# Optimization experiments

Hardware: AMD Instinct MI355X
Metric: run time of the kernel (lower is better)

The kernel has to match this reference:

```python
import jax, jax.numpy as jnp
import numpy as np

EMBED_DIM = 1024
NUM_HEADS = 16
HEAD_DIM = EMBED_DIM // NUM_HEADS
B, T = 4, 2048


def setup_inputs() -> dict:
    key = jax.random.key(0)
    ks = jax.random.split(key, 5)
    s = 1.0 / np.sqrt(EMBED_DIM)
    x = jax.random.normal(ks[0], (B, T, EMBED_DIM), dtype=jnp.float32)
    attention_mask = jnp.ones((B, 1, 1, T), dtype=jnp.int32)
    # torch Linear weights: qkv (3E, E), out (E, E); store transposed for x @ W
    W_qkv = jax.random.uniform(ks[1], (EMBED_DIM, 3 * EMBED_DIM), jnp.float32, -s, s)
    b_qkv = jax.random.uniform(ks[2], (3 * EMBED_DIM,), jnp.float32, -s, s)
    W_out = jax.random.uniform(ks[3], (EMBED_DIM, EMBED_DIM), jnp.float32, -s, s)
    b_out = jax.random.uniform(ks[4], (EMBED_DIM,), jnp.float32, -s, s)
    return {"x": x, "attention_mask": attention_mask,
            "W_qkv": W_qkv, "b_qkv": b_qkv, "W_out": W_out, "b_out": b_out}


def reference(x, attention_mask, W_qkv, b_qkv, W_out, b_out):
    Bq, Tq, E = x.shape
    qkv = x @ W_qkv + b_qkv                              # [B,T,3E]
    qkv = qkv.reshape(Bq, Tq, 3, NUM_HEADS, HEAD_DIM)
    qkv = jnp.transpose(qkv, (2, 0, 3, 1, 4))            # [3,B,H,T,d]
    q, k, v = qkv[0], qkv[1], qkv[2]
    scores = jnp.einsum('bhqd,bhkd->bhqk', q, k) / jnp.sqrt(
        jnp.asarray(HEAD_DIM, x.dtype))                  # [B,H,T,T]
    scores = jnp.where(attention_mask == 0, jnp.asarray(-jnp.inf, x.dtype), scores)
    attn = jax.nn.softmax(scores, axis=-1)
    ctx = jnp.einsum('bhqk,bhkd->bhqd', attn, v)         # [B,H,T,d]
    ctx = jnp.transpose(ctx, (0, 2, 1, 3)).reshape(Bq, Tq, E)
    return ctx @ W_out + b_out
```

## Files before the change

### kernel.cpp

```cpp
#include <hip/hip_runtime.h>
#include <hip/hip_bf16.h>
#include <stdint.h>


typedef __attribute__((ext_vector_type(8))) short short8;
typedef __attribute__((ext_vector_type(4))) float f32x4;
typedef __attribute__((ext_vector_type(16))) float f32x16;
typedef __attribute__((ext_vector_type(4))) unsigned short ushort4_t;
typedef __attribute__((ext_vector_type(8))) unsigned short ushort8_t;

#define SEQ 2048
#define EDIM 1024
#define QSCALE 0.18033688011112042f

__device__ __forceinline__ unsigned short f2bf(float x) {
  union { float f; uint32_t u; } v; v.f = x;
  uint32_t r = v.u + 0x7fffu + ((v.u >> 16) & 1u);
  return (unsigned short)(r >> 16);
}

__device__ __forceinline__ uint32_t cvtpk(float lo, float hi) {
  uint32_t r;
  asm("v_cvt_pk_bf16_f32 %0, %1, %2" : "=v"(r) : "v"(lo), "v"(hi));
  return r;
}

__device__ __forceinline__ float exp2_raw(float x) {
  float r;
  asm("v_exp_f32 %0, %1" : "=v"(r) : "v"(x));
  return r;
}

__device__ __forceinline__ void gload_lds16(const void* g, void* l) {
  typedef __attribute__((address_space(1))) const unsigned int gu32;
  typedef __attribute__((address_space(3))) unsigned int lu32;
  __builtin_amdgcn_global_load_lds((gu32*)g, (lu32*)l, 16, 0, 0);
}

__global__ void k_cvt(const float* __restrict__ in,
                      unsigned short* __restrict__ out, int n8) {
  int i = blockIdx.x * blockDim.x + threadIdx.x;
  if (i >= n8) return;
  const float4* p = ((const float4*)in) + (size_t)i * 2;
  float4 a = p[0], b = p[1];
  ushort8_t v;
  v[0] = f2bf(a.x); v[1] = f2bf(a.y); v[2] = f2bf(a.z); v[3] = f2bf(a.w);
  v[4] = f2bf(b.x); v[5] = f2bf(b.y); v[6] = f2bf(b.z); v[7] = f2bf(b.w);
  ((ushort8_t*)out)[i] = v;
}

__global__ void k_transpose(const float* __restrict__ W,
                            unsigned short* __restrict__ Wt, int K, int N) {
  __shared__ float tile[32][33];
  int c0 = blockIdx.x * 32;
  int r0 = blockIdx.y * 32;
  int tx = threadIdx.x & 31, ty = threadIdx.x >> 5;
#pragma unroll
  for (int i = 0; i < 4; ++i) {
    int r = ty + i * 8;
    tile[r][tx] = W[(size_t)(r0 + r) * N + c0 + tx];
  }
  __syncthreads();
#pragma unroll
  for (int i = 0; i < 4; ++i) {
    int r = ty + i * 8;
    Wt[(size_t)(c0 + r) * K + r0 + tx] = f2bf(tile[tx][r]);
  }
}

template <int EPI, int NBX>
__global__ __launch_bounds__(256, 2) void k_gemm(
    const unsigned short* __restrict__ A, const unsigned short* __restrict__ Bt,
    const float* __restrict__ bias, unsigned short* __restrict__ Qo,
    unsigned short* __restrict__ Ko, unsigned short* __restrict__ VTo,
    float* __restrict__ Out) {
  __shared__ unsigned short As[128 * 32];
  __shared__ unsigned short Bs[128 * 32];
  const int tid = threadIdx.x;
  const int lane = tid & 63, wid = tid >> 6;
  const int wr = wid >> 1, wc = wid & 1;
  const int g = lane >> 4, r = lane & 15;
  const int lid = blockIdx.y * NBX + blockIdx.x;
  const int total = NBX * gridDim.y;
  const int id = (lid & 7) * (total >> 3) + (lid >> 3);
  const int m0 = (id / NBX) * 128, n0 = (id % NBX) * 128;

  f32x4 zero4 = {0.f, 0.f, 0.f, 0.f};
  f32x4 acc[4][4];
#pragma unroll
  for (int mi = 0; mi < 4; ++mi)
#pragma unroll
    for (int ni = 0; ni < 4; ++ni) acc[mi][ni] = zero4;

  for (int kt = 0; kt < 1024; kt += 32) {
#pragma unroll
    for (int i = 0; i < 2; ++i) {
      int seg = i * 256 + tid;
      int row = seg >> 2, sl = seg & 3;
      gload_lds16(A + (size_t)(m0 + row) * 1024 + kt + sl * 8,
                  (char*)As + (i * 256 + wid * 64) * 16);
      gload_lds16(Bt + (size_t)(n0 + row) * 1024 + kt + sl * 8,
                  (char*)Bs + (i * 256 + wid * 64) * 16);
    }
    __syncthreads();
    short8 af[4], bf[4];
#pragma unroll
    for (int mi = 0; mi < 4; ++mi)
      af[mi] = *(const short8*)&As[(wr * 64 + mi * 16 + r) * 32 + g * 8];
#pragma unroll
    for (int ni = 0; ni < 4; ++ni)
      bf[ni] = *(const short8*)&Bs[(wc * 64 + ni * 16 + r) * 32 + g * 8];
#pragma unroll
    for (int mi = 0; mi < 4; ++mi)
#pragma unroll
      for (int ni = 0; ni < 4; ++ni)
        acc[mi][ni] = __builtin_amdgcn_mfma_f32_16x16x32_bf16(
            af[mi], bf[ni], acc[mi][ni], 0, 0, 0);
    __syncthreads();
  }

#pragma unroll
  for (int mi = 0; mi < 4; ++mi) {
#pragma unroll
    for (int ni = 0; ni < 4; ++ni) {
      const int n = n0 + wc * 64 + ni * 16 + r;
      const float bv = bias[n];
      const int mbase = m0 + wr * 64 + mi * 16 + g * 4;
      if (EPI == 0) {
        const int sec = n >> 10, e = n & 1023, h = e >> 6, dd = e & 63;
        const int b = mbase >> 11, t = mbase & 2047;
        if (sec == 2) {
          ushort4_t pk;
#pragma unroll
          for (int j = 0; j < 4; ++j) pk[j] = f2bf(acc[mi][ni][j] + bv);
          *(ushort4_t*)&VTo[(((size_t)b * 16 + h) * 64 + dd) * 2048 + t] = pk;
        } else {
          unsigned short* dst = (sec == 0) ? Qo : Ko;
          const float scl = (sec == 0) ? QSCALE : 1.0f;
#pragma unroll
          for (int j = 0; j < 4; ++j)
            dst[(((size_t)b * 16 + h) * 2048 + t + j) * 64 + dd] =
                f2bf((acc[mi][ni][j] + bv) * scl);
        }
      } else {
#pragma unroll
        for (int j = 0; j < 4; ++j)
          Out[(size_t)(mbase + j) * 1024 + n] = acc[mi][ni][j] + bv;
      }
    }
  }
}

__global__ __launch_bounds__(256, 4) void k_attn(
    const unsigned short* __restrict__ Qg, const unsigned short* __restrict__ Kg,
    const unsigned short* __restrict__ VTg, const int* __restrict__ maskp,
    unsigned short* __restrict__ ctx) {
  __shared__ unsigned short Ks[2][64 * 64];
  __shared__ unsigned short Vs[2][64 * 64];
  const int tid = threadIdx.x, lane = tid & 63, wid = tid >> 6;
  const int q = lane & 31, hi = lane >> 5;
  const int id = blockIdx.x;
  const int slot = id >> 3;
  const int bh = (id & 7) * 8 + (slot >> 4);
  const int b = bh >> 4, h = bh & 15;
  const int q0 = (slot & 15) * 128 + wid * 32;
  const int qr = q0 + q;

  const unsigned short* Qb = Qg + (size_t)bh * SEQ * 64;
  const unsigned short* Kb = Kg + (size_t)bh * SEQ * 64;
  const unsigned short* Vb = VTg + (size_t)bh * 64 * SEQ;
  const int* mb = maskp + b * SEQ;

  const int r0_ = tid >> 3, sl0_ = (tid & 7) ^ (r0_ & 7);
  const int r1_ = (256 + tid) >> 3, sl1_ = ((256 + tid) & 7) ^ (r1_ & 7);
  const unsigned short* kp0 = Kb + r0_ * 64 + sl0_ * 8;
  const unsigned short* kp1 = Kb + r1_ * 64 + sl1_ * 8;
  const unsigned short* vp0 = Vb + (size_t)r0_ * SEQ + sl0_ * 8;
  const unsigned short* vp1 = Vb + (size_t)r1_ * SEQ + sl1_ * 8;
  char* kbase = (char*)Ks[0] + wid * 1024;
  char* vbase = (char*)Vs[0] + wid * 1024;

  auto STAGE = [&](int buf) {
    const int bo = buf * 8192;
    gload_lds16(kp0, kbase + bo);
    gload_lds16(kp1, kbase + bo + 4096);
    gload_lds16(vp0, vbase + bo);
    gload_lds16(vp1, vbase + bo + 4096);
    kp0 += 64 * 64; kp1 += 64 * 64;
    vp0 += 64; vp1 += 64;
  };

  short8 qf[4];
#pragma unroll
  for (int ds = 0; ds < 4; ++ds)
    qf[ds] = *(const short8*)&Qb[(size_t)qr * 64 + ds * 16 + hi * 8];

  short8 onesf;
#pragma unroll
  for (int j = 0; j < 8; ++j) onesf[j] = (short)0x3F80;

  f32x16 z16 = {0.f,0.f,0.f,0.f,0.f,0.f,0.f,0.f,0.f,0.f,0.f,0.f,0.f,0.f,0.f,0.f};
  f32x16 o0 = z16, o1 = z16;
  f32x16 osum = z16;
  const int kb4 = hi * 4;

  STAGE(0);
  const int* mptr = mb + lane;
  int mv = mptr[0];
  mptr += 64;

  for (int t = 0; t < 32; ++t) {
    const int cur = t & 1;
    __syncthreads();
    int mvn = 1;
    if (t < 31) {
      STAGE(cur ^ 1);
      mvn = mptr[0];
      mptr += 64;
    }
    const unsigned long long bits = __ballot(mv != 0);
    mv = mvn;

    const char* KsB = (const char*)Ks[cur];
    const char* VsB = (const char*)Vs[cur];
    f32x16 c0 = z16, c1 = z16;
    __builtin_amdgcn_s_setprio(1);
#pragma unroll
    for (int ds = 0; ds < 4; ++ds) {
      const int sl = ds * 2 + hi;
      short8 ka0 = *(const short8*)(KsB + q * 128 + ((sl ^ (q & 7)) * 16));
      short8 ka1 = *(const short8*)(KsB + (32 + q) * 128 + ((sl ^ (q & 7)) * 16));
      c0 = __builtin_amdgcn_mfma_f32_32x32x16_bf16(ka0, qf[ds], c0, 0, 0, 0);
      c1 = __builtin_amdgcn_mfma_f32_32x32x16_bf16(ka1, qf[ds], c1, 0, 0, 0);
    }
    __builtin_amdgcn_s_setprio(0);

#pragma unroll
    for (int i = 0; i < 16; ++i) {
      c0[i] = exp2_raw(c0[i]);
      c1[i] = exp2_raw(c1[i]);
    }
    if (bits != ~0ull) {
#pragma unroll
      for (int i = 0; i < 16; ++i) {
        const int k0 = (i & 3) + 8 * (i >> 2) + kb4;
        if (!((bits >> k0) & 1)) c0[i] = 0.f;
        if (!((bits >> (k0 + 32)) & 1)) c1[i] = 0.f;
      }
    }

    short8 pf[4];
#pragma unroll
    for (int sub = 0; sub < 2; ++sub) {
      uint32_t w[8];
#pragma unroll
      for (int j = 0; j < 8; ++j)
        w[j] = sub ? cvtpk(c1[2 * j], c1[2 * j + 1])
                   : cvtpk(c0[2 * j], c0[2 * j + 1]);
      asm("v_permlane32_swap_b32 %0, %1" : "+v"(w[0]), "+v"(w[2]));
      asm("v_permlane32_swap_b32 %0, %1" : "+v"(w[1]), "+v"(w[3]));
      asm("v_permlane32_swap_b32 %0, %1" : "+v"(w[4]), "+v"(w[6]));
      asm("v_permlane32_swap_b32 %0, %1" : "+v"(w[5]), "+v"(w[7]));
      union { uint32_t u[4]; short8 s; } ua, ub;
      ua.u[0] = w[0]; ua.u[1] = w[1]; ua.u[2] = w[2]; ua.u[3] = w[3];
      ub.u[0] = w[4]; ub.u[1] = w[5]; ub.u[2] = w[6]; ub.u[3] = w[7];
      pf[sub * 2] = ua.s;
      pf[sub * 2 + 1] = ub.s;
    }

    __builtin_amdgcn_s_setprio(1);
#pragma unroll
    for (int ks = 0; ks < 4; ++ks) {
      const int sl = ks * 2 + hi;
      short8 va0 = *(const short8*)(VsB + q * 128 + ((sl ^ (q & 7)) * 16));
      short8 va1 = *(const short8*)(VsB + (32 + q) * 128 + ((sl ^ (q & 7)) * 16));
      o0 = __builtin_amdgcn_mfma_f32_32x32x16_bf16(va0, pf[ks], o0, 0, 0, 0);
      o1 = __builtin_amdgcn_mfma_f32_32x32x16_bf16(va1, pf[ks], o1, 0, 0, 0);
      osum = __builtin_amdgcn_mfma_f32_32x32x16_bf16(onesf, pf[ks], osum,
                                                     0, 0, 0);
    }
    __builtin_amdgcn_s_setprio(0);
  }

  const float inv = 1.f / osum[0];
#pragma unroll
  for (int ns = 0; ns < 2; ++ns) {
#pragma unroll
    for (int g_ = 0; g_ < 4; ++g_) {
      ushort4_t v4;
#pragma unroll
      for (int e = 0; e < 4; ++e) {
        const float val = (ns ? o1[g_ * 4 + e] : o0[g_ * 4 + e]) * inv;
        v4[e] = f2bf(val);
      }
      *(ushort4_t*)&ctx[((size_t)b * SEQ + qr) * 1024 + h * 64 + ns * 32 +
                        g_ * 8 + hi * 4] = v4;
    }
  }
}

extern "C" void kernel_launch(void* const* d_in, const int* in_sizes, int n_in,
                              void* d_out, int out_size, void* d_ws,
                              size_t ws_size, hipStream_t stream) {
  const float* x = (const float*)d_in[0];
  const int* mask = (const int*)d_in[1];
  const float* Wqkv = (const float*)d_in[2];
  const float* bqkv = (const float*)d_in[3];
  const float* Wout = (const float*)d_in[4];
  const float* bout = (const float*)d_in[5];
  float* out = (float*)d_out;

  unsigned short* ws = (unsigned short*)d_ws;
  unsigned short* xb = ws;
  unsigned short* wqt = ws + 8388608;
  unsigned short* wot = ws + 11534336;
  unsigned short* Q = ws + 12582912;
  unsigned short* K = ws + 20971520;
  unsigned short* VT = ws + 29360128;
  unsigned short* ctx = xb;

  k_cvt<<<4096, 256, 0, stream>>>(x, xb, 1048576);
  k_transpose<<<dim3(96, 32), 256, 0, stream>>>(Wqkv, wqt, 1024, 3072);
  k_transpose<<<dim3(32, 32), 256, 0, stream>>>(Wout, wot, 1024, 1024);
  k_gemm<0, 24><<<dim3(24, 64), 256, 0, stream>>>(xb, wqt, bqkv, Q, K, VT,
                                                  nullptr);
  k_attn<<<1024, 256, 0, stream>>>(Q, K, VT, mask, ctx);
  k_gemm<1, 8><<<dim3(8, 64), 256, 0, stream>>>(ctx, wot, bout, nullptr,
                                                nullptr, nullptr, out);
}
```

Baseline: 208.9 us.

## Software-pipeline attention PV with next QK, triple-buffer K/V, fuse prep kernels

The attention loop now runs the P·V MFMAs for the previous tile right after the QK^T MFMAs of the current tile. This overlaps the exp/convert/permlane work with matrix ops, and K/V LDS buffers grow from two to three stages so the previous V tile stays resident. Separately, the bf16 conversion of x and the two weight transposes are merged into one k_prep launch to cut launch overhead. The cost is more LDS per block, which may reduce occupancy, plus extra registers for carrying the P fragments across iterations.

```diff
diff --git a/kernel.cpp b/kernel.cpp
--- a/kernel.cpp
+++ b/kernel.cpp
@@ -37,24 +37,32 @@
   __builtin_amdgcn_global_load_lds((gu32*)g, (lu32*)l, 16, 0, 0);
 }
 
-__global__ void k_cvt(const float* __restrict__ in,
-                      unsigned short* __restrict__ out, int n8) {
-  int i = blockIdx.x * blockDim.x + threadIdx.x;
-  if (i >= n8) return;
-  const float4* p = ((const float4*)in) + (size_t)i * 2;
-  float4 a = p[0], b = p[1];
-  ushort8_t v;
-  v[0] = f2bf(a.x); v[1] = f2bf(a.y); v[2] = f2bf(a.z); v[3] = f2bf(a.w);
-  v[4] = f2bf(b.x); v[5] = f2bf(b.y); v[6] = f2bf(b.z); v[7] = f2bf(b.w);
-  ((ushort8_t*)out)[i] = v;
-}
-
-__global__ void k_transpose(const float* __restrict__ W,
-                            unsigned short* __restrict__ Wt, int K, int N) {
+__global__ void k_prep(const float* __restrict__ x,
+                       unsigned short* __restrict__ xb,
+                       const float* __restrict__ Wq,
+                       unsigned short* __restrict__ wqt,
+                       const float* __restrict__ Wo,
+                       unsigned short* __restrict__ wot) {
   __shared__ float tile[32][33];
-  int c0 = blockIdx.x * 32;
-  int r0 = blockIdx.y * 32;
-  int tx = threadIdx.x & 31, ty = threadIdx.x >> 5;
+  const int id = blockIdx.x;
+  if (id < 4096) {
+    const int i = id * 256 + threadIdx.x;
+    const float4* p = ((const float4*)x) + (size_t)i * 2;
+    float4 a = p[0], b = p[1];
+    ushort8_t v;
+    v[0] = f2bf(a.x); v[1] = f2bf(a.y); v[2] = f2bf(a.z); v[3] = f2bf(a.w);
+    v[4] = f2bf(b.x); v[5] = f2bf(b.y); v[6] = f2bf(b.z); v[7] = f2bf(b.w);
+    ((ushort8_t*)xb)[i] = v;
+    return;
+  }
+  const float* W;
+  unsigned short* Wt;
+  int N, bx, by;
+  if (id < 7168) { W = Wq; Wt = wqt; N = 3072; bx = (id - 4096) % 96; by = (id - 4096) / 96; }
+  else           { W = Wo; Wt = wot; N = 1024; bx = (id - 7168) % 32; by = (id - 7168) / 32; }
+  const int K = 1024;
+  const int c0 = bx * 32, r0 = by * 32;
+  const int tx = threadIdx.x & 31, ty = threadIdx.x >> 5;
 #pragma unroll
   for (int i = 0; i < 4; ++i) {
     int r = ty + i * 8;
@@ -155,8 +163,8 @@
     const unsigned short* __restrict__ Qg, const unsigned short* __restrict__ Kg,
     const unsigned short* __restrict__ VTg, const int* __restrict__ maskp,
     unsigned short* __restrict__ ctx) {
-  __shared__ unsigned short Ks[2][64 * 64];
-  __shared__ unsigned short Vs[2][64 * 64];
+  __shared__ unsigned short Ks[3][64 * 64];
+  __shared__ unsigned short Vs[3][64 * 64];
   const int tid = threadIdx.x, lane = tid & 63, wid = tid >> 6;
   const int q = lane & 31, hi = lane >> 5;
   const int id = blockIdx.x;
@@ -180,8 +188,7 @@
   char* kbase = (char*)Ks[0] + wid * 1024;
   char* vbase = (char*)Vs[0] + wid * 1024;
 
-  auto STAGE = [&](int buf) {
-    const int bo = buf * 8192;
+  auto STAGE = [&](int bo) {
     gload_lds16(kp0, kbase + bo);
     gload_lds16(kp1, kbase + bo + 4096);
     gload_lds16(vp0, vbase + bo);
@@ -202,27 +209,31 @@
   f32x16 z16 = {0.f,0.f,0.f,0.f,0.f,0.f,0.f,0.f,0.f,0.f,0.f,0.f,0.f,0.f,0.f,0.f};
   f32x16 o0 = z16, o1 = z16;
   f32x16 osum = z16;
+  short8 pfp[4];
+#pragma unroll
+  for (int j = 0; j < 4; ++j) pfp[j] = onesf;
   const int kb4 = hi * 4;
 
   STAGE(0);
   const int* mptr = mb + lane;
   int mv = mptr[0];
   mptr += 64;
+  int cur = 0, nxt = 1, prv = 2;
 
   for (int t = 0; t < 32; ++t) {
-    const int cur = t & 1;
     __syncthreads();
     int mvn = 1;
     if (t < 31) {
-      STAGE(cur ^ 1);
+      STAGE(nxt * 8192);
       mvn = mptr[0];
       mptr += 64;
     }
     const unsigned long long bits = __ballot(mv != 0);
     mv = mvn;
 
-    const char* KsB = (const char*)Ks[cur];
-    const char* VsB = (const char*)Vs[cur];
+    const char* KsB = (const char*)Ks[0] + cur * 8192;
+    const char* VsP = (const char*)Vs[0] + prv * 8192;
+
     f32x16 c0 = z16, c1 = z16;
     __builtin_amdgcn_s_setprio(1);
 #pragma unroll
@@ -233,6 +244,19 @@
       c0 = __builtin_amdgcn_mfma_f32_32x32x16_bf16(ka0, qf[ds], c0, 0, 0, 0);
       c1 = __builtin_amdgcn_mfma_f32_32x32x16_bf16(ka1, qf[ds], c1, 0, 0, 0);
     }
+
+    if (t > 0) {
+#pragma unroll
+      for (int ks = 0; ks < 4; ++ks) {
+        const int sl = ks * 2 + hi;
+        short8 va0 = *(const short8*)(VsP + q * 128 + ((sl ^ (q & 7)) * 16));
+        short8 va1 = *(const short8*)(VsP + (32 + q) * 128 + ((sl ^ (q & 7)) * 16));
+        o0 = __builtin_amdgcn_mfma_f32_32x32x16_bf16(va0, pfp[ks], o0, 0, 0, 0);
+        o1 = __builtin_amdgcn_mfma_f32_32x32x16_bf16(va1, pfp[ks], o1, 0, 0, 0);
+        osum = __builtin_amdgcn_mfma_f32_32x32x16_bf16(onesf, pfp[ks], osum,
+                                                       0, 0, 0);
+      }
+    }
     __builtin_amdgcn_s_setprio(0);
 
 #pragma unroll
@@ -249,7 +273,6 @@
       }
     }
 
-    short8 pf[4];
 #pragma unroll
     for (int sub = 0; sub < 2; ++sub) {
       uint32_t w[8];
@@ -264,19 +287,24 @@
       union { uint32_t u[4]; short8 s; } ua, ub;
       ua.u[0] = w[0]; ua.u[1] = w[1]; ua.u[2] = w[2]; ua.u[3] = w[3];
       ub.u[0] = w[4]; ub.u[1] = w[5]; ub.u[2] = w[6]; ub.u[3] = w[7];
-      pf[sub * 2] = ua.s;
-      pf[sub * 2 + 1] = ub.s;
-    }
-
+      pfp[sub * 2] = ua.s;
+      pfp[sub * 2 + 1] = ub.s;
+    }
+
+    prv = cur; cur = nxt; nxt = (nxt == 2) ? 0 : nxt + 1;
+  }
+
+  {
+    const char* VsP = (const char*)Vs[0] + prv * 8192;
     __builtin_amdgcn_s_setprio(1);
 #pragma unroll
     for (int ks = 0; ks < 4; ++ks) {
       const int sl = ks * 2 + hi;
-      short8 va0 = *(const short8*)(VsB + q * 128 + ((sl ^ (q & 7)) * 16));
-      short8 va1 = *(const short8*)(VsB + (32 + q) * 128 + ((sl ^ (q & 7)) * 16));
-      o0 = __builtin_amdgcn_mfma_f32_32x32x16_bf16(va0, pf[ks], o0, 0, 0, 0);
-      o1 = __builtin_amdgcn_mfma_f32_32x32x16_bf16(va1, pf[ks], o1, 0, 0, 0);
-      osum = __builtin_amdgcn_mfma_f32_32x32x16_bf16(onesf, pf[ks], osum,
+      short8 va0 = *(const short8*)(VsP + q * 128 + ((sl ^ (q & 7)) * 16));
+      short8 va1 = *(const short8*)(VsP + (32 + q) * 128 + ((sl ^ (q & 7)) * 16));
+      o0 = __builtin_amdgcn_mfma_f32_32x32x16_bf16(va0, pfp[ks], o0, 0, 0, 0);
+      o1 = __builtin_amdgcn_mfma_f32_32x32x16_bf16(va1, pfp[ks], o1, 0, 0, 0);
+      osum = __builtin_amdgcn_mfma_f32_32x32x16_bf16(onesf, pfp[ks], osum,
                                                      0, 0, 0);
     }
     __builtin_amdgcn_s_setprio(0);
@@ -319,9 +347,7 @@
   unsigned short* VT = ws + 29360128;
   unsigned short* ctx = xb;
 
-  k_cvt<<<4096, 256, 0, stream>>>(x, xb, 1048576);
-  k_transpose<<<dim3(96, 32), 256, 0, stream>>>(Wqkv, wqt, 1024, 3072);
-  k_transpose<<<dim3(32, 32), 256, 0, stream>>>(Wout, wot, 1024, 1024);
+  k_prep<<<8192, 256, 0, stream>>>(x, xb, Wqkv, wqt, Wout, wot);
   k_gemm<0, 24><<<dim3(24, 64), 256, 0, stream>>>(xb, wqt, bqkv, Q, K, VT,
                                                   nullptr);
   k_attn<<<1024, 256, 0, stream>>>(Q, K, VT, mask, ctx);
```

Measured after the change: 202.5 us. 3.1% less time.

## Merge prep kernels into one launch and use 512-thread attention blocks

Applied to the files above, without the earlier changes.

Merges the x conversion and both weight transposes into one k_prep launch, dispatching on block index, to cut two kernel launches. The attention kernel now runs 8 waves per block covering 256 queries. The K/V tile staging is spread across the 8 waves, so each thread issues half as many global-to-LDS loads and every staged K/V tile is shared by twice as many query rows. The cost is larger blocks and fewer of them (512), which may reduce scheduling flexibility and occupancy, and the launch bound of 512 threads with 4 blocks per unit puts more pressure on registers.

```diff
diff --git a/kernel.cpp b/kernel.cpp
--- a/kernel.cpp
+++ b/kernel.cpp
@@ -37,24 +37,32 @@
   __builtin_amdgcn_global_load_lds((gu32*)g, (lu32*)l, 16, 0, 0);
 }
 
-__global__ void k_cvt(const float* __restrict__ in,
-                      unsigned short* __restrict__ out, int n8) {
-  int i = blockIdx.x * blockDim.x + threadIdx.x;
-  if (i >= n8) return;
-  const float4* p = ((const float4*)in) + (size_t)i * 2;
-  float4 a = p[0], b = p[1];
-  ushort8_t v;
-  v[0] = f2bf(a.x); v[1] = f2bf(a.y); v[2] = f2bf(a.z); v[3] = f2bf(a.w);
-  v[4] = f2bf(b.x); v[5] = f2bf(b.y); v[6] = f2bf(b.z); v[7] = f2bf(b.w);
-  ((ushort8_t*)out)[i] = v;
-}
-
-__global__ void k_transpose(const float* __restrict__ W,
-                            unsigned short* __restrict__ Wt, int K, int N) {
+__global__ void k_prep(const float* __restrict__ x,
+                       unsigned short* __restrict__ xb,
+                       const float* __restrict__ Wq,
+                       unsigned short* __restrict__ wqt,
+                       const float* __restrict__ Wo,
+                       unsigned short* __restrict__ wot) {
   __shared__ float tile[32][33];
-  int c0 = blockIdx.x * 32;
-  int r0 = blockIdx.y * 32;
-  int tx = threadIdx.x & 31, ty = threadIdx.x >> 5;
+  const int id = blockIdx.x;
+  if (id < 4096) {
+    const int i = id * 256 + threadIdx.x;
+    const float4* p = ((const float4*)x) + (size_t)i * 2;
+    float4 a = p[0], b = p[1];
+    ushort8_t v;
+    v[0] = f2bf(a.x); v[1] = f2bf(a.y); v[2] = f2bf(a.z); v[3] = f2bf(a.w);
+    v[4] = f2bf(b.x); v[5] = f2bf(b.y); v[6] = f2bf(b.z); v[7] = f2bf(b.w);
+    ((ushort8_t*)xb)[i] = v;
+    return;
+  }
+  const float* W;
+  unsigned short* Wt;
+  int N, bx, by;
+  if (id < 7168) { W = Wq; Wt = wqt; N = 3072; bx = (id - 4096) % 96; by = (id - 4096) / 96; }
+  else           { W = Wo; Wt = wot; N = 1024; bx = (id - 7168) % 32; by = (id - 7168) / 32; }
+  const int K = 1024;
+  const int c0 = bx * 32, r0 = by * 32;
+  const int tx = threadIdx.x & 31, ty = threadIdx.x >> 5;
 #pragma unroll
   for (int i = 0; i < 4; ++i) {
     int r = ty + i * 8;
@@ -151,7 +159,7 @@
   }
 }
 
-__global__ __launch_bounds__(256, 4) void k_attn(
+__global__ __launch_bounds__(512, 4) void k_attn(
     const unsigned short* __restrict__ Qg, const unsigned short* __restrict__ Kg,
     const unsigned short* __restrict__ VTg, const int* __restrict__ maskp,
     unsigned short* __restrict__ ctx) {
@@ -161,9 +169,9 @@
   const int q = lane & 31, hi = lane >> 5;
   const int id = blockIdx.x;
   const int slot = id >> 3;
-  const int bh = (id & 7) * 8 + (slot >> 4);
+  const int bh = (id & 7) * 8 + (slot >> 3);
   const int b = bh >> 4, h = bh & 15;
-  const int q0 = (slot & 15) * 128 + wid * 32;
+  const int q0 = (slot & 7) * 256 + wid * 32;
   const int qr = q0 + q;
 
   const unsigned short* Qb = Qg + (size_t)bh * SEQ * 64;
@@ -172,22 +180,17 @@
   const int* mb = maskp + b * SEQ;
 
   const int r0_ = tid >> 3, sl0_ = (tid & 7) ^ (r0_ & 7);
-  const int r1_ = (256 + tid) >> 3, sl1_ = ((256 + tid) & 7) ^ (r1_ & 7);
   const unsigned short* kp0 = Kb + r0_ * 64 + sl0_ * 8;
-  const unsigned short* kp1 = Kb + r1_ * 64 + sl1_ * 8;
   const unsigned short* vp0 = Vb + (size_t)r0_ * SEQ + sl0_ * 8;
-  const unsigned short* vp1 = Vb + (size_t)r1_ * SEQ + sl1_ * 8;
   char* kbase = (char*)Ks[0] + wid * 1024;
   char* vbase = (char*)Vs[0] + wid * 1024;
 
   auto STAGE = [&](int buf) {
     const int bo = buf * 8192;
     gload_lds16(kp0, kbase + bo);
-    gload_lds16(kp1, kbase + bo + 4096);
     gload_lds16(vp0, vbase + bo);
-    gload_lds16(vp1, vbase + bo + 4096);
-    kp0 += 64 * 64; kp1 += 64 * 64;
-    vp0 += 64; vp1 += 64;
+    kp0 += 64 * 64;
+    vp0 += 64;
   };
 
   short8 qf[4];
@@ -319,12 +322,10 @@
   unsigned short* VT = ws + 29360128;
   unsigned short* ctx = xb;
 
-  k_cvt<<<4096, 256, 0, stream>>>(x, xb, 1048576);
-  k_transpose<<<dim3(96, 32), 256, 0, stream>>>(Wqkv, wqt, 1024, 3072);
-  k_transpose<<<dim3(32, 32), 256, 0, stream>>>(Wout, wot, 1024, 1024);
+  k_prep<<<8192, 256, 0, stream>>>(x, xb, Wqkv, wqt, Wout, wot);
   k_gemm<0, 24><<<dim3(24, 64), 256, 0, stream>>>(xb, wqt, bqkv, Q, K, VT,
                                                   nullptr);
-  k_attn<<<1024, 256, 0, stream>>>(Q, K, VT, mask, ctx);
+  k_attn<<<512, 512, 0, stream>>>(Q, K, VT, mask, ctx);
   k_gemm<1, 8><<<dim3(8, 64), 256, 0, stream>>>(ctx, wot, bout, nullptr,
                                                 nullptr, nullptr, out);
 }
```

After: 199.3 us. -4.6%, faster.
